# Kernel optimization log

Measured on AMD Instinct MI355X. Metric: run time of the kernel, lower is better.

The kernel has to match this reference:

```python
import jax, jax.numpy as jnp
import numpy as np

K = 3          # cfg.KNN_UP
CHUNK = 2048   # point chunk for brute-force KNN
BN_EPS = 1e-5


def knn_interp(vox_c, vox_f, pt_c):
    """Inverse-distance k-NN interpolation of voxel features onto points.
    vox_c: [Nv,3] voxel centers; vox_f: [Nv,C]; pt_c: [Np,3]. Returns [Np,C]."""
    Np = pt_c.shape[0]

    def chunk_fn(pc):  # pc: [CHUNK,3]
        d2 = jnp.sum((pc[:, None, :] - vox_c[None, :, :]) ** 2, axis=-1)  # [CHUNK,Nv]
        neg_d2, idx = jax.lax.top_k(-d2, K)                               # k nearest
        d = jnp.sqrt(jnp.maximum(-neg_d2, 0.0))
        w = 1.0 / (d + 1e-8)
        w = w / jnp.sum(w, axis=-1, keepdims=True)                        # [CHUNK,K]
        return jnp.sum(vox_f[idx] * w[..., None], axis=1)                 # [CHUNK,C]

    out = jax.lax.map(chunk_fn, pt_c.reshape(Np // CHUNK, CHUNK, 3))
    return out.reshape(Np, vox_f.shape[-1])


def bn1d(x, gamma, beta):
    # BatchNorm1d in training mode, applied per decomposed batch item (as in
    # the original per-sample list comprehension): stats over the point dim.
    mu = jnp.mean(x, axis=0, keepdims=True)
    var = jnp.var(x, axis=0, keepdims=True)
    return gamma * (x - mu) * jax.lax.rsqrt(var + BN_EPS) + beta


def level_forward(vox_c, vox_f, pt_c, gamma, beta):
    f = jax.vmap(knn_interp, in_axes=(0, 0, 0))(vox_c, vox_f, pt_c)  # [B,Np,C]
    return jax.vmap(lambda xf: bn1d(xf, gamma, beta))(f)


def setup_inputs() -> dict:
    key = jax.random.key(0)
    ks = jax.random.split(key, 16)
    B, Np = 2, 32768
    SCENE = 50.0  # spread coordinates over a ~50m scene
    nvs = [2048, 6144, 16384, 32768]
    chs = [256, 128, 96, 96]
    inp = {"pt_c": jax.random.uniform(ks[0], (B, Np, 3), jnp.float32) * SCENE}
    for i, (nv, c) in enumerate(zip(nvs, chs), start=1):
        inp[f"vox_c{i}"] = jax.random.uniform(ks[2 * i - 1], (B, nv, 3), jnp.float32) * SCENE
        inp[f"vox_f{i}"] = jax.random.normal(ks[2 * i], (B, nv, c), jnp.float32)
        inp[f"gamma{i}"] = jnp.ones((c,), jnp.float32)
        inp[f"beta{i}"] = jnp.zeros((c,), jnp.float32)
    return inp


def reference(pt_c, vox_c1, vox_f1, gamma1, beta1,
              vox_c2, vox_f2, gamma2, beta2,
              vox_c3, vox_f3, gamma3, beta3,
              vox_c4, vox_f4, gamma4, beta4):
    # voxel_to_point: per-level KNN upsampling of decoder voxel features to
    # the raw point cloud, followed by per-sample BatchNorm1d.
    f1 = level_forward(vox_c1, vox_f1, pt_c, gamma1, beta1)
    f2 = level_forward(vox_c2, vox_f2, pt_c, gamma2, beta2)
    f3 = level_forward(vox_c3, vox_f3, pt_c, gamma3, beta3)
    f4 = level_forward(vox_c4, vox_f4, pt_c, gamma4, beta4)
    return (f1, f2, f3, f4)
```

## Files before the change

kernel.cpp:

```cpp
#include <hip/hip_runtime.h>
#include <cfloat>
#include <climits>
#include <cstdint>

#define NPOINTS 32768
#define NBATCH  2
#define NLEV    4
#define NJOB    5
#define PG      16
#define PCELLS  (PG*PG*PG)
#define NPB     128
#define NBLK    (NPOINTS / NPB)

struct BinJob {
  const float* coords;
  int* cnt; int* start; int* cur;
  float4* sorted;
  int G, ncells, N;
  float invh;
};
struct BinParams { BinJob job[NJOB]; };

struct Level {
  const float4* sorted;
  const int*    start;
  int*          idxo;
  float*        wo;
  int G, ncells, Nv;
  float h, invh;
};
struct Params { Level lv[NLEV]; };

__device__ __forceinline__ int cell1d(float x, float invh, int G) {
  int c = (int)(x * invh);
  return min(max(c, 0), G - 1);
}

__global__ __launch_bounds__(256) void zero_kernel(int* __restrict__ p, int n)
{
  int i = blockIdx.x * 256 + threadIdx.x;
  if (i < n) p[i] = 0;
}

__global__ __launch_bounds__(256) void count_kernel(BinParams prm)
{
  const BinJob J = prm.job[blockIdx.z];
  int v = blockIdx.x * 256 + threadIdx.x;
  int b = blockIdx.y;
  if (v >= J.N) return;
  const float* p = J.coords + ((size_t)b * J.N + v) * 3;
  int cx = cell1d(p[0], J.invh, J.G), cy = cell1d(p[1], J.invh, J.G), cz = cell1d(p[2], J.invh, J.G);
  atomicAdd(&J.cnt[b * J.ncells + (cz * J.G + cy) * J.G + cx], 1);
}

__global__ __launch_bounds__(1024) void scan_kernel(BinParams prm)
{
  const BinJob J = prm.job[blockIdx.y];
  const int b = blockIdx.x, t = threadIdx.x;
  const int ncells = J.ncells;
  const int* c  = J.cnt + (size_t)b * ncells;
  int* st = J.start + (size_t)b * (ncells + 1);
  int* cu = J.cur + (size_t)b * ncells;
  __shared__ int part[1024];
  const int chunk = (ncells + 1023) / 1024;
  const int lo = t * chunk, hi = min(lo + chunk, ncells);
  int s = 0;
  for (int i = lo; i < hi; ++i) s += c[i];
  part[t] = s;
  __syncthreads();
  for (int off = 1; off < 1024; off <<= 1) {
    int v = (t >= off) ? part[t - off] : 0;
    __syncthreads();
    part[t] += v;
    __syncthreads();
  }
  int base = (t > 0) ? part[t - 1] : 0;
  for (int i = lo; i < hi; ++i) { st[i] = base; cu[i] = base; base += c[i]; }
  if (t == 1023) st[ncells] = part[1023];
}

__global__ __launch_bounds__(256) void scatter_kernel(BinParams prm)
{
  const BinJob J = prm.job[blockIdx.z];
  int v = blockIdx.x * 256 + threadIdx.x;
  int b = blockIdx.y;
  if (v >= J.N) return;
  const float* p = J.coords + ((size_t)b * J.N + v) * 3;
  float x = p[0], y = p[1], z = p[2];
  int cx = cell1d(x, J.invh, J.G), cy = cell1d(y, J.invh, J.G), cz = cell1d(z, J.invh, J.G);
  int pos = atomicAdd(&J.cur[b * J.ncells + (cz * J.G + cy) * J.G + cx], 1);
  J.sorted[(size_t)b * J.N + pos] = make_float4(x, y, z, __int_as_float(v));
}

__global__ __launch_bounds__(256) void query_kernel(
    const float4* __restrict__ psorted, Params prm)
{
  const int l = blockIdx.y, b = blockIdx.z;
  const Level L = prm.lv[l];
  const int tid = threadIdx.x;
  const int q = tid & 3;
  const int sp = blockIdx.x * 64 + (tid >> 2);
  float4 pt = psorted[(size_t)b * NPOINTS + sp];
  const float px = pt.x, py = pt.y, pz = pt.z;
  const int p = __float_as_int(pt.w);
  const int G = L.G;
  const float h = L.h;

  const int cx = cell1d(px, L.invh, G);
  const int cy = cell1d(py, L.invh, G);
  const int cz = cell1d(pz, L.invh, G);
  const float fx = px - cx * h, fy = py - cy * h, fz = pz - cz * h;
  float m = fminf(fminf(fminf(fx, h - fx), fminf(fy, h - fy)), fminf(fz, h - fz));
  m = fmaxf(m, 0.f);

  const int* start     = L.start  + (size_t)b * (L.ncells + 1);
  const float4* sorted = L.sorted + (size_t)b * L.Nv;

  float b0 = FLT_MAX, b1 = FLT_MAX, b2 = FLT_MAX;
  int   i0 = INT_MAX, i1 = INT_MAX, i2 = INT_MAX;

  auto ins = [&](float d2, int vi) {
    if (d2 < b2 || (d2 == b2 && vi < i2)) {
      if (d2 < b1 || (d2 == b1 && vi < i1)) {
        b2 = b1; i2 = i1;
        if (d2 < b0 || (d2 == b0 && vi < i0)) { b1 = b0; i1 = i0; b0 = d2; i0 = vi; }
        else                                  { b1 = d2; i1 = vi; }
      } else { b2 = d2; i2 = vi; }
    }
  };
  auto cand = [&](int k) {
    float4 vv = sorted[k];
    int vi = __float_as_int(vv.w);
    float dx = px - vv.x, dy = py - vv.y, dz = pz - vv.z;
    float d2 = __fadd_rn(__fadd_rn(__fmul_rn(dx, dx), __fmul_rn(dy, dy)),
                         __fmul_rn(dz, dz));
    ins(d2, vi);
  };
  auto scan_range = [&](int ks, int ke) {
    for (int k = ks + q; k < ke; k += 4) cand(k);
  };

  const int rmax = max(max(cx, G - 1 - cx), max(max(cy, G - 1 - cy), max(cz, G - 1 - cz)));
  for (int rho = 0; rho <= rmax; ++rho) {
    if (rho >= 1) {
      float bm = fminf(b2, __shfl_xor(b2, 1));
      bm = fminf(bm, __shfl_xor(bm, 2));
      float dmin = fmaxf((rho - 1) * h + m, 0.f);
      if (dmin * dmin * 0.99999f > bm) break;
    }
    const int z0 = max(cz - rho, 0), z1 = min(cz + rho, G - 1);
    const int y0 = max(cy - rho, 0), y1 = min(cy + rho, G - 1);
    for (int iz = z0; iz <= z1; ++iz) {
      const int adz = abs(iz - cz);
      for (int iy = y0; iy <= y1; ++iy) {
        const int ady = max(adz, abs(iy - cy));
        const int row = (iz * G + iy) * G;
        if (ady == rho) {
          const int x0 = max(cx - rho, 0), x1 = min(cx + rho, G - 1);
          scan_range(start[row + x0], start[row + x1 + 1]);
        } else {
          const int xl = cx - rho, xr = cx + rho;
          if (xl >= 0)     scan_range(start[row + xl], start[row + xl + 1]);
          if (xr <= G - 1) scan_range(start[row + xr], start[row + xr + 1]);
        }
      }
    }
  }

  #pragma unroll
  for (int mask = 1; mask <= 2; mask <<= 1) {
    float c0 = __shfl_xor(b0, mask), c1 = __shfl_xor(b1, mask), c2 = __shfl_xor(b2, mask);
    int   j0 = __shfl_xor(i0, mask), j1 = __shfl_xor(i1, mask), j2 = __shfl_xor(i2, mask);
    ins(c0, j0); ins(c1, j1); ins(c2, j2);
  }

  if (q == 0) {
    float w0 = 1.0f / (sqrtf(b0) + 1e-8f);
    float w1 = 1.0f / (sqrtf(b1) + 1e-8f);
    float w2 = 1.0f / (sqrtf(b2) + 1e-8f);
    float ws = (w0 + w1) + w2;
    size_t o = ((size_t)b * NPOINTS + p) * 3;
    L.idxo[o] = i0; L.idxo[o + 1] = i1; L.idxo[o + 2] = i2;
    L.wo[o] = w0 / ws; L.wo[o + 1] = w1 / ws; L.wo[o + 2] = w2 / ws;
  }
}

template <int C, int BDIM>
__global__ __launch_bounds__(BDIM) void interp_kernel(
    const float* __restrict__ voxf, const int* __restrict__ idxo,
    const float* __restrict__ wo, float* __restrict__ out,
    float* __restrict__ psum, float* __restrict__ psq, int Nv)
{
  constexpr int C4 = C / 4;
  constexpr int R  = BDIM / C4;
  const int b = blockIdx.y, blk = blockIdx.x;
  const int tid = threadIdx.x;
  const int r = tid / C4, c4 = tid - r * C4;
  const float4* fb = (const float4*)(voxf + (size_t)b * Nv * C);
  float4* ob = (float4*)(out + (size_t)b * NPOINTS * C);
  const int p0 = blk * NPB;

  float4 s = make_float4(0, 0, 0, 0), q = make_float4(0, 0, 0, 0);
  for (int p = p0 + r; p < p0 + NPB; p += R) {
    size_t pg = ((size_t)b * NPOINTS + p) * 3;
    int   ia = idxo[pg], ib = idxo[pg + 1], ic = idxo[pg + 2];
    float wa = wo[pg],   wb = wo[pg + 1],   wc = wo[pg + 2];
    float4 fa = fb[(size_t)ia * C4 + c4];
    float4 f2 = fb[(size_t)ib * C4 + c4];
    float4 fc = fb[(size_t)ic * C4 + c4];
    float4 o;
    o.x = wa * fa.x + wb * f2.x + wc * fc.x;
    o.y = wa * fa.y + wb * f2.y + wc * fc.y;
    o.z = wa * fa.z + wb * f2.z + wc * fc.z;
    o.w = wa * fa.w + wb * f2.w + wc * fc.w;
    ob[(size_t)p * C4 + c4] = o;
    s.x += o.x; s.y += o.y; s.z += o.z; s.w += o.w;
    q.x += o.x * o.x; q.y += o.y * o.y; q.z += o.z * o.z; q.w += o.w * o.w;
  }

  __shared__ float4 ls[BDIM];
  ls[tid] = s;
  __syncthreads();
  if (r == 0) {
    float4 tot = s;
    #pragma unroll
    for (int rr = 1; rr < R; ++rr) {
      float4 v = ls[c4 + rr * C4];
      tot.x += v.x; tot.y += v.y; tot.z += v.z; tot.w += v.w;
    }
    ((float4*)psum)[((size_t)b * NBLK + blk) * C4 + c4] = tot;
  }
  __syncthreads();
  ls[tid] = q;
  __syncthreads();
  if (r == 0) {
    float4 tot = q;
    #pragma unroll
    for (int rr = 1; rr < R; ++rr) {
      float4 v = ls[c4 + rr * C4];
      tot.x += v.x; tot.y += v.y; tot.z += v.z; tot.w += v.w;
    }
    ((float4*)psq)[((size_t)b * NBLK + blk) * C4 + c4] = tot;
  }
}

__global__ __launch_bounds__(256) void bn_stats_kernel(
    const float* __restrict__ psum, const float* __restrict__ psq,
    const float* __restrict__ gamma, const float* __restrict__ beta,
    float* __restrict__ scale, float* __restrict__ shift, int C, float invN)
{
  const int c = blockIdx.x, b = blockIdx.y, t = threadIdx.x;
  float s = 0.f, q = 0.f;
  for (int k = t; k < NBLK; k += 256) {
    s += psum[((size_t)b * NBLK + k) * C + c];
    q += psq[((size_t)b * NBLK + k) * C + c];
  }
  __shared__ float ss[256], qs[256];
  ss[t] = s; qs[t] = q;
  __syncthreads();
  for (int o = 128; o > 0; o >>= 1) {
    if (t < o) { ss[t] += ss[t + o]; qs[t] += qs[t + o]; }
    __syncthreads();
  }
  if (t == 0) {
    float mu  = ss[0] * invN;
    float var = fmaxf(qs[0] * invN - mu * mu, 0.f);
    float sc  = gamma[c] * rsqrtf(var + 1e-5f);
    scale[b * C + c] = sc;
    shift[b * C + c] = beta[c] - mu * sc;
  }
}

__global__ __launch_bounds__(256) void bn_apply_kernel(
    float* __restrict__ out, const float* __restrict__ scale,
    const float* __restrict__ shift, int C, int NpC)
{
  const int e = blockIdx.x * 256 + threadIdx.x;
  const int npc4 = NpC >> 2, c4n = C >> 2;
  const int b = e / npc4;
  const int rem = e - b * npc4;
  const int c4 = rem % c4n;
  float4 v  = ((float4*)out)[e];
  float4 sc = ((const float4*)scale)[b * c4n + c4];
  float4 sh = ((const float4*)shift)[b * c4n + c4];
  v.x = fmaf(v.x, sc.x, sh.x);
  v.y = fmaf(v.y, sc.y, sh.y);
  v.z = fmaf(v.z, sc.z, sh.z);
  v.w = fmaf(v.w, sc.w, sh.w);
  ((float4*)out)[e] = v;
}

extern "C" void kernel_launch(void* const* d_in, const int* in_sizes, int n_in,
                              void* d_out, int out_size, void* d_ws, size_t ws_size,
                              hipStream_t stream)
{
  const float* ptc = (const float*)d_in[0];
  static const int    Cs[4]     = {256, 128, 96, 96};
  static const int    Nvs[4]    = {2048, 6144, 16384, 32768};
  static const int    Gs[4]     = {10, 14, 18, 22};
  static const size_t outOff[4] = {0, 16777216, 25165824, 31457280};

  size_t off = 0;
  auto carve = [&](size_t bytes) {
    off = (off + 255) & ~(size_t)255;
    size_t o = off; off += bytes; return o;
  };
  char* w = (char*)d_ws;

  int nc[NJOB];
  for (int l = 0; l < 4; ++l) nc[l] = Gs[l] * Gs[l] * Gs[l];
  nc[4] = PCELLS;
  int Ns[NJOB] = {Nvs[0], Nvs[1], Nvs[2], Nvs[3], NPOINTS};
  int Gj[NJOB] = {Gs[0], Gs[1], Gs[2], Gs[3], PG};

  int totcnt = 0;
  for (int j = 0; j < NJOB; ++j) totcnt += nc[j];
  int* cntbase = (int*)(w + carve((size_t)NBATCH * totcnt * 4));

  float4* sortedj[NJOB]; int* cntj[NJOB]; int* sttj[NJOB]; int* curj[NJOB];
  {
    int acc = 0;
    for (int j = 0; j < NJOB; ++j) {
      cntj[j] = cntbase + (size_t)NBATCH * acc;
      acc += nc[j];
    }
  }
  for (int j = 0; j < NJOB; ++j) {
    sortedj[j] = (float4*)(w + carve((size_t)NBATCH * Ns[j] * 16));
    sttj[j]    = (int*)   (w + carve((size_t)NBATCH * (nc[j] + 1) * 4));
    curj[j]    = (int*)   (w + carve((size_t)NBATCH * nc[j] * 4));
  }
  int*   idxo  = (int*)  (w + carve((size_t)NLEV * NBATCH * NPOINTS * 3 * 4));
  float* wo    = (float*)(w + carve((size_t)NLEV * NBATCH * NPOINTS * 3 * 4));
  float* psum  = (float*)(w + carve((size_t)NBATCH * NBLK * 256 * 4));
  float* psq   = (float*)(w + carve((size_t)NBATCH * NBLK * 256 * 4));
  float* scale = (float*)(w + carve((size_t)NBATCH * 256 * 4));
  float* shift = (float*)(w + carve((size_t)NBATCH * 256 * 4));

  BinParams bp;
  for (int j = 0; j < NJOB; ++j) {
    BinJob& J = bp.job[j];
    J.coords = (j < 4) ? (const float*)d_in[1 + 4 * j] : ptc;
    J.cnt = cntj[j]; J.start = sttj[j]; J.cur = curj[j]; J.sorted = sortedj[j];
    J.G = Gj[j]; J.ncells = nc[j]; J.N = Ns[j];
    J.invh = Gj[j] / 50.0f;
  }

  Params prm;
  for (int l = 0; l < 4; ++l) {
    Level& L = prm.lv[l];
    L.sorted = sortedj[l]; L.start = sttj[l];
    L.idxo = idxo + (size_t)l * NBATCH * NPOINTS * 3;
    L.wo   = wo   + (size_t)l * NBATCH * NPOINTS * 3;
    L.G = Gs[l]; L.ncells = nc[l]; L.Nv = Nvs[l];
    L.h = 50.0f / Gs[l]; L.invh = Gs[l] / 50.0f;
  }

  const int zn = NBATCH * totcnt;
  zero_kernel<<<(zn + 255) / 256, 256, 0, stream>>>(cntbase, zn);
  count_kernel<<<dim3((NPOINTS + 255) / 256, NBATCH, NJOB), 256, 0, stream>>>(bp);
  scan_kernel<<<dim3(NBATCH, NJOB), 1024, 0, stream>>>(bp);
  scatter_kernel<<<dim3((NPOINTS + 255) / 256, NBATCH, NJOB), 256, 0, stream>>>(bp);

  query_kernel<<<dim3(NPOINTS / 64, NLEV, NBATCH), 256, 0, stream>>>(sortedj[4], prm);

  for (int l = 0; l < 4; ++l) {
    const float* voxf  = (const float*)d_in[2 + 4 * l];
    const float* gamma = (const float*)d_in[3 + 4 * l];
    const float* beta  = (const float*)d_in[4 + 4 * l];
    const int C = Cs[l], Nv = Nvs[l];
    float* outl = (float*)d_out + outOff[l];
    const int* idl = idxo + (size_t)l * NBATCH * NPOINTS * 3;
    const float* wl = wo  + (size_t)l * NBATCH * NPOINTS * 3;

    if (C == 256)
      interp_kernel<256, 256><<<dim3(NBLK, NBATCH), 256, 0, stream>>>(
          voxf, idl, wl, outl, psum, psq, Nv);
    else if (C == 128)
      interp_kernel<128, 256><<<dim3(NBLK, NBATCH), 256, 0, stream>>>(
          voxf, idl, wl, outl, psum, psq, Nv);
    else
      interp_kernel<96, 240><<<dim3(NBLK, NBATCH), 240, 0, stream>>>(
          voxf, idl, wl, outl, psum, psq, Nv);

    bn_stats_kernel<<<dim3(C, NBATCH), 256, 0, stream>>>(
        psum, psq, gamma, beta, scale, shift, C, 1.0f / NPOINTS);

    const int n4 = NBATCH * NPOINTS * C / 4;
    bn_apply_kernel<<<n4 / 256, 256, 0, stream>>>(
        (float*)outl, scale, shift, C, NPOINTS * C);
  }
}
```

Before: 338.9 us.

## Split KNN query into fixed 3x3x3 phase plus compacted tail, merge BN apply

The KNN query now runs a fast first pass that scans only the 27 neighbouring cells and writes results directly when the third-nearest neighbour is guaranteed to lie inside that shell. Points that fail the check are added to a compacted list with an atomic counter, and a tail kernel runs the full expanding-shell search on just those points. This is meant to cut the divergence and loop overhead the ring search pays for the common case, at the cost of an extra launch and atomics. The four per-level BN apply launches are also merged into one kernel, with per-level scale/shift buffers.

```diff
diff --git a/kernel.cpp b/kernel.cpp
--- a/kernel.cpp
+++ b/kernel.cpp
@@ -30,6 +30,11 @@
   float h, invh;
 };
 struct Params { Level lv[NLEV]; };
+
+struct ApplyParams {
+  const float* scale[NLEV];
+  const float* shift[NLEV];
+};
 
 __device__ __forceinline__ int cell1d(float x, float invh, int G) {
   int c = (int)(x * invh);
@@ -92,14 +97,113 @@
   J.sorted[(size_t)b * J.N + pos] = make_float4(x, y, z, __int_as_float(v));
 }
 
-__global__ __launch_bounds__(256) void query_kernel(
-    const float4* __restrict__ psorted, Params prm)
+__global__ __launch_bounds__(256) void phase1_kernel(
+    const float4* __restrict__ psorted, Params prm,
+    unsigned* __restrict__ taillist, int* __restrict__ tailcnt)
 {
   const int l = blockIdx.y, b = blockIdx.z;
   const Level L = prm.lv[l];
   const int tid = threadIdx.x;
   const int q = tid & 3;
   const int sp = blockIdx.x * 64 + (tid >> 2);
+  float4 pt = psorted[(size_t)b * NPOINTS + sp];
+  const float px = pt.x, py = pt.y, pz = pt.z;
+  const int p = __float_as_int(pt.w);
+  const int G = L.G;
+  const float h = L.h;
+
+  const int cx = cell1d(px, L.invh, G);
+  const int cy = cell1d(py, L.invh, G);
+  const int cz = cell1d(pz, L.invh, G);
+  const float fx = px - cx * h, fy = py - cy * h, fz = pz - cz * h;
+  float m = fminf(fminf(fminf(fx, h - fx), fminf(fy, h - fy)), fminf(fz, h - fz));
+  m = fmaxf(m, 0.f);
+
+  const int* start     = L.start  + (size_t)b * (L.ncells + 1);
+  const float4* sorted = L.sorted + (size_t)b * L.Nv;
+
+  float b0 = FLT_MAX, b1 = FLT_MAX, b2 = FLT_MAX;
+  int   i0 = INT_MAX, i1 = INT_MAX, i2 = INT_MAX;
+
+  auto ins = [&](float d2, int vi) {
+    if (d2 < b2 || (d2 == b2 && vi < i2)) {
+      if (d2 < b1 || (d2 == b1 && vi < i1)) {
+        b2 = b1; i2 = i1;
+        if (d2 < b0 || (d2 == b0 && vi < i0)) { b1 = b0; i1 = i0; b0 = d2; i0 = vi; }
+        else                                  { b1 = d2; i1 = vi; }
+      } else { b2 = d2; i2 = vi; }
+    }
+  };
+  auto cand = [&](int k) {
+    float4 vv = sorted[k];
+    int vi = __float_as_int(vv.w);
+    float dx = px - vv.x, dy = py - vv.y, dz = pz - vv.z;
+    float d2 = __fadd_rn(__fadd_rn(__fmul_rn(dx, dx), __fmul_rn(dy, dy)),
+                         __fmul_rn(dz, dz));
+    ins(d2, vi);
+  };
+
+  {
+    const int x0 = max(cx - 1, 0), x1 = min(cx + 1, G - 1);
+    int ks9[9], ke9[9];
+    #pragma unroll
+    for (int i = 0; i < 9; ++i) {
+      const int dz = i / 3 - 1, dy = i % 3 - 1;
+      const int iz = cz + dz, iy = cy + dy;
+      const bool ok = (iz >= 0) && (iz < G) && (iy >= 0) && (iy < G);
+      const int row = (iz * G + iy) * G;
+      const int sa = ok ? (row + x0) : 0;
+      const int sb = ok ? (row + x1 + 1) : 0;
+      int a = start[sa], e = start[sb];
+      if (!ok) { a = 0; e = 0; }
+      ks9[i] = a; ke9[i] = e;
+    }
+    #pragma unroll
+    for (int i = 0; i < 9; ++i)
+      for (int k = ks9[i] + q; k < ke9[i]; k += 4) cand(k);
+  }
+
+  #pragma unroll
+  for (int mask = 1; mask <= 2; mask <<= 1) {
+    float c0 = __shfl_xor(b0, mask), c1 = __shfl_xor(b1, mask), c2 = __shfl_xor(b2, mask);
+    int   j0 = __shfl_xor(i0, mask), j1 = __shfl_xor(i1, mask), j2 = __shfl_xor(i2, mask);
+    ins(c0, j0); ins(c1, j1); ins(c2, j2);
+  }
+
+  float dmin = h + m;
+  bool contained = (dmin * dmin * 0.99999f > b2);
+
+  if (q == 0) {
+    if (contained) {
+      float w0 = 1.0f / (sqrtf(b0) + 1e-8f);
+      float w1 = 1.0f / (sqrtf(b1) + 1e-8f);
+      float w2 = 1.0f / (sqrtf(b2) + 1e-8f);
+      float ws = (w0 + w1) + w2;
+      size_t o = ((size_t)b * NPOINTS + p) * 3;
+      L.idxo[o] = i0; L.idxo[o + 1] = i1; L.idxo[o + 2] = i2;
+      L.wo[o] = w0 / ws; L.wo[o + 1] = w1 / ws; L.wo[o + 2] = w2 / ws;
+    } else {
+      int slot = atomicAdd(tailcnt, 1);
+      taillist[slot] = (unsigned)sp | ((unsigned)l << 15) | ((unsigned)b << 17);
+    }
+  }
+}
+
+__global__ __launch_bounds__(256) void tail_kernel(
+    const float4* __restrict__ psorted, Params prm,
+    const unsigned* __restrict__ taillist, const int* __restrict__ tailcnt)
+{
+  const int tid = threadIdx.x;
+  const int q = tid & 3;
+  const int ent = blockIdx.x * 64 + (tid >> 2);
+  const int n = *tailcnt;
+  if (ent >= n) return;
+
+  unsigned e = taillist[ent];
+  const int sp = e & 0x7fff;
+  const int l  = (e >> 15) & 3;
+  const int b  = (e >> 17) & 1;
+  const Level L = prm.lv[l];
   float4 pt = psorted[(size_t)b * NPOINTS + sp];
   const float px = pt.x, py = pt.y, pz = pt.z;
   const int p = __float_as_int(pt.w);
@@ -156,8 +260,8 @@
         const int ady = max(adz, abs(iy - cy));
         const int row = (iz * G + iy) * G;
         if (ady == rho) {
-          const int x0 = max(cx - rho, 0), x1 = min(cx + rho, G - 1);
-          scan_range(start[row + x0], start[row + x1 + 1]);
+          const int xa = max(cx - rho, 0), xb = min(cx + rho, G - 1);
+          scan_range(start[row + xa], start[row + xb + 1]);
         } else {
           const int xl = cx - rho, xr = cx + rho;
           if (xl >= 0)     scan_range(start[row + xl], start[row + xl + 1]);
@@ -271,18 +375,26 @@
   }
 }
 
-__global__ __launch_bounds__(256) void bn_apply_kernel(
-    float* __restrict__ out, const float* __restrict__ scale,
-    const float* __restrict__ shift, int C, int NpC)
+#define O1 4194304
+#define O2 6291456
+#define O3 7864320
+__global__ __launch_bounds__(256) void bn_apply_all_kernel(
+    float* __restrict__ out, ApplyParams ap)
 {
   const int e = blockIdx.x * 256 + threadIdx.x;
-  const int npc4 = NpC >> 2, c4n = C >> 2;
-  const int b = e / npc4;
-  const int rem = e - b * npc4;
-  const int c4 = rem % c4n;
+  int l, base, C4;
+  if (e < O1)      { l = 0; base = 0;  C4 = 64; }
+  else if (e < O2) { l = 1; base = O1; C4 = 32; }
+  else if (e < O3) { l = 2; base = O2; C4 = 24; }
+  else             { l = 3; base = O3; C4 = 24; }
+  const int local = e - base;
+  const int npc4 = NPOINTS * C4;
+  const int b = local / npc4;
+  const int rem = local - b * npc4;
+  const int c4 = rem % C4;
   float4 v  = ((float4*)out)[e];
-  float4 sc = ((const float4*)scale)[b * c4n + c4];
-  float4 sh = ((const float4*)shift)[b * c4n + c4];
+  float4 sc = ((const float4*)ap.scale[l])[b * C4 + c4];
+  float4 sh = ((const float4*)ap.shift[l])[b * C4 + c4];
   v.x = fmaf(v.x, sc.x, sh.x);
   v.y = fmaf(v.y, sc.y, sh.y);
   v.z = fmaf(v.z, sc.z, sh.z);
@@ -315,7 +427,8 @@
 
   int totcnt = 0;
   for (int j = 0; j < NJOB; ++j) totcnt += nc[j];
-  int* cntbase = (int*)(w + carve((size_t)NBATCH * totcnt * 4));
+  int* cntbase = (int*)(w + carve(((size_t)NBATCH * totcnt + 1) * 4));
+  int* tailcnt = cntbase + (size_t)NBATCH * totcnt;
 
   float4* sortedj[NJOB]; int* cntj[NJOB]; int* sttj[NJOB]; int* curj[NJOB];
   {
@@ -330,12 +443,16 @@
     sttj[j]    = (int*)   (w + carve((size_t)NBATCH * (nc[j] + 1) * 4));
     curj[j]    = (int*)   (w + carve((size_t)NBATCH * nc[j] * 4));
   }
-  int*   idxo  = (int*)  (w + carve((size_t)NLEV * NBATCH * NPOINTS * 3 * 4));
-  float* wo    = (float*)(w + carve((size_t)NLEV * NBATCH * NPOINTS * 3 * 4));
-  float* psum  = (float*)(w + carve((size_t)NBATCH * NBLK * 256 * 4));
-  float* psq   = (float*)(w + carve((size_t)NBATCH * NBLK * 256 * 4));
-  float* scale = (float*)(w + carve((size_t)NBATCH * 256 * 4));
-  float* shift = (float*)(w + carve((size_t)NBATCH * 256 * 4));
+  int*      idxo   = (int*)     (w + carve((size_t)NLEV * NBATCH * NPOINTS * 3 * 4));
+  float*    wo     = (float*)   (w + carve((size_t)NLEV * NBATCH * NPOINTS * 3 * 4));
+  unsigned* taillist = (unsigned*)(w + carve((size_t)NLEV * NBATCH * NPOINTS * 4));
+  float*    psum   = (float*)   (w + carve((size_t)NBATCH * NBLK * 256 * 4));
+  float*    psq    = (float*)   (w + carve((size_t)NBATCH * NBLK * 256 * 4));
+  float*    scale4[4]; float* shift4[4];
+  for (int l = 0; l < 4; ++l) {
+    scale4[l] = (float*)(w + carve((size_t)NBATCH * 256 * 4));
+    shift4[l] = (float*)(w + carve((size_t)NBATCH * 256 * 4));
+  }
 
   BinParams bp;
   for (int j = 0; j < NJOB; ++j) {
@@ -356,13 +473,19 @@
     L.h = 50.0f / Gs[l]; L.invh = Gs[l] / 50.0f;
   }
 
-  const int zn = NBATCH * totcnt;
+  ApplyParams ap;
+  for (int l = 0; l < 4; ++l) { ap.scale[l] = scale4[l]; ap.shift[l] = shift4[l]; }
+
+  const int zn = NBATCH * totcnt + 1;
   zero_kernel<<<(zn + 255) / 256, 256, 0, stream>>>(cntbase, zn);
   count_kernel<<<dim3((NPOINTS + 255) / 256, NBATCH, NJOB), 256, 0, stream>>>(bp);
   scan_kernel<<<dim3(NBATCH, NJOB), 1024, 0, stream>>>(bp);
   scatter_kernel<<<dim3((NPOINTS + 255) / 256, NBATCH, NJOB), 256, 0, stream>>>(bp);
 
-  query_kernel<<<dim3(NPOINTS / 64, NLEV, NBATCH), 256, 0, stream>>>(sortedj[4], prm);
+  phase1_kernel<<<dim3(NPOINTS / 64, NLEV, NBATCH), 256, 0, stream>>>(
+      sortedj[4], prm, taillist, tailcnt);
+  tail_kernel<<<(NLEV * NBATCH * NPOINTS) / 64, 256, 0, stream>>>(
+      sortedj[4], prm, taillist, tailcnt);
 
   for (int l = 0; l < 4; ++l) {
     const float* voxf  = (const float*)d_in[2 + 4 * l];
@@ -384,10 +507,9 @@
           voxf, idl, wl, outl, psum, psq, Nv);
 
     bn_stats_kernel<<<dim3(C, NBATCH), 256, 0, stream>>>(
-        psum, psq, gamma, beta, scale, shift, C, 1.0f / NPOINTS);
-
-    const int n4 = NBATCH * NPOINTS * C / 4;
-    bn_apply_kernel<<<n4 / 256, 256, 0, stream>>>(
-        (float*)outl, scale, shift, C, NPOINTS * C);
-  }
-}
+        psum, psq, gamma, beta, scale4[l], shift4[l], C, 1.0f / NPOINTS);
+  }
+
+  const int n4tot = 9437184;
+  bn_apply_all_kernel<<<n4tot / 256, 256, 0, stream>>>((float*)d_out, ap);
+}
```

Measured after the change: 391.9 us. 1.16x slower.
